# Kernel optimization log

Measured on AMD Instinct MI355X. Metric: run time of the kernel, lower is better.

## Reference

```python
import jax, jax.numpy as jnp
import numpy as np

D_MODEL, D_STATE, D_CONV, EXPAND = 2048, 16, 4, 2
D_INNER = D_MODEL * EXPAND
DT_RANK = D_MODEL // 16
B_SZ, SEQ = 2, 1024
WS = 0.02  # weight init scale for numerical stability


def setup_inputs() -> dict:
    key = jax.random.key(0)
    ks = jax.random.split(key, 14)
    rn = lambda k, s, sc=WS: jax.random.normal(k, s, dtype=jnp.float32) * sc
    return {
        "u": rn(ks[0], (B_SZ, SEQ, D_MODEL), 1.0),
        "w_in": rn(ks[1], (2 * D_INNER, D_MODEL)),
        "b_in": rn(ks[2], (2 * D_INNER,)),
        "w_out": rn(ks[3], (D_MODEL, D_INNER)),
        "b_out": rn(ks[4], (D_MODEL,)),
        "w_dt": rn(ks[5], (D_INNER, DT_RANK)),
        "b_dt": rn(ks[6], (D_INNER,)),
        "w_xdt": rn(ks[7], (DT_RANK, D_INNER)),
        "w_xb": rn(ks[8], (D_STATE, D_INNER)),
        "w_xc": rn(ks[9], (D_STATE, D_INNER)),
        "conv_w": rn(ks[10], (D_INNER, 1, D_CONV), 0.2),
        "conv_b": rn(ks[11], (D_INNER,), 0.1),
        "A_log": jnp.log(jax.random.uniform(ks[12], (D_INNER, D_STATE), minval=0.5, maxval=8.0)),
        "D_param": rn(ks[13], (D_INNER,), 1.0),
    }


def reference(u, w_in, b_in, w_out, b_out, w_dt, b_dt, w_xdt, w_xb, w_xc, conv_w, conv_b, A_log, D_param):
    B, L, _ = u.shape
    # in_proj and split into x, z   [B, L, D_INNER] each
    xz = u @ w_in.T + b_in
    x, z = jnp.split(xz, 2, axis=-1)
    # causal depthwise conv1d (torch pads both sides D_CONV-1 then slices [:L] == left pad)
    xt = x.transpose(0, 2, 1)  # [B, D_INNER, L]
    conv = jax.lax.conv_general_dilated(
        xt, conv_w, window_strides=(1,), padding=[(D_CONV - 1, 0)],
        feature_group_count=D_INNER, dimension_numbers=("NCH", "OIH", "NCH"))
    x = jax.nn.silu((conv + conv_b[None, :, None]).transpose(0, 2, 1))  # [B, L, D_INNER]
    # SSM parameters
    dt = jax.nn.softplus((x @ w_xdt.T) @ w_dt.T + b_dt)  # [B, L, D_INNER]
    Bm = x @ w_xb.T  # [B, L, D_STATE]
    Cm = x @ w_xc.T  # [B, L, D_STATE]
    A = -jnp.exp(A_log.astype(jnp.float32))  # [D_INNER, D_STATE]

    def step(h, inp):
        dt_t, B_t, C_t, x_t = inp  # [B,D_INNER], [B,N], [B,N], [B,D_INNER]
        dA = jnp.exp(dt_t[..., None] * A)                         # [B, D_INNER, N]
        h = h * dA + x_t[..., None] * (dt_t[..., None] * B_t[:, None, :])
        y = jnp.einsum("bdn,bn->bd", h, C_t) + D_param * x_t
        return h, y

    h0 = jnp.zeros((B, D_INNER, D_STATE), dtype=x.dtype)
    _, ys = jax.lax.scan(step, h0, (dt.transpose(1, 0, 2), Bm.transpose(1, 0, 2),
                                    Cm.transpose(1, 0, 2), x.transpose(1, 0, 2)))
    y = ys.transpose(1, 0, 2) * jax.nn.silu(z)  # [B, L, D_INNER]
    return y @ w_out.T + b_out
```

## Files before the change

### kernel.cpp

```cpp
#include <hip/hip_runtime.h>
#include <hip/hip_bf16.h>


#define DEV __device__ __forceinline__

typedef __attribute__((ext_vector_type(8))) __bf16 bf16x8;
typedef __attribute__((ext_vector_type(4))) float f32x4;
typedef unsigned int u32;

DEV float bf2f(__hip_bfloat16 x) { return __bfloat162float(x); }
DEV __hip_bfloat16 f2bf(float x) { return __float2bfloat16(x); }
DEV float bfu2f(unsigned short u) {
    union { u32 i; float f; } c; c.i = ((u32)u) << 16; return c.f;
}
DEV unsigned short f2bfu(float x) {
    __hip_bfloat16 h = __float2bfloat16(x);
    return *reinterpret_cast<unsigned short*>(&h);
}
DEV float softplusf(float v) { return v > 20.f ? v : log1pf(__expf(v)); }
DEV float siluf(float v) { return v / (1.f + __expf(-v)); }

DEV void storeOut(float* C, size_t off, float v) { C[off] = v; }
DEV void storeOut(__hip_bfloat16* C, size_t off, float v) { C[off] = f2bf(v); }

DEV void async16(void* lds, const void* g) {
    __builtin_amdgcn_global_load_lds(
        (const __attribute__((address_space(1))) u32*)(unsigned long long)g,
        (__attribute__((address_space(3))) u32*)(u32)(unsigned long long)lds,
        16, 0, 0);
}

template <int CTRL>
DEV float dppadd(float v) {
    int x = __builtin_amdgcn_update_dpp(
        0, __builtin_bit_cast(int, v), CTRL, 0xF, 0xF, true);
    return v + __builtin_bit_cast(float, x);
}

__global__ __launch_bounds__(512, 2) void gemm256_bt(
    const __hip_bfloat16* __restrict__ A, int lda,
    const __hip_bfloat16* __restrict__ W, int ldw,
    const float* __restrict__ bias,
    __hip_bfloat16* __restrict__ C, int ldc, int K)
{
    __shared__ __align__(16) unsigned short As[4][256 * 32];
    __shared__ __align__(16) unsigned short Bs[4][256 * 32];

    const int t    = threadIdx.x;
    const int nwg  = gridDim.x * gridDim.y;
    const int orig = blockIdx.y * gridDim.x + blockIdx.x;
    const int swz  = (orig & 7) * (nwg >> 3) + (orig >> 3);
    const int mBase = (swz / gridDim.x) * 256;
    const int nBase = (swz % gridDim.x) * 256;

    const int wave = t >> 6;
    const int lane = t & 63;
    const int wm   = (wave >> 2) * 128;
    const int wn   = (wave & 3) * 64;
    const int ln15 = lane & 15;
    const int quad = lane >> 4;
    const int kof  = quad * 8;

    f32x4 acc[8][4];
    const f32x4 vzero = {0.f, 0.f, 0.f, 0.f};
#pragma unroll
    for (int i = 0; i < 8; ++i)
#pragma unroll
        for (int j = 0; j < 4; ++j) acc[i][j] = vzero;

    auto stage = [&](int buf, int k0, int half) {
        const int idx = half * 512 + t;
        const int le  = (idx * 8) ^ (((idx >> 3) & 3) << 3);
        const int r   = le >> 5;
        const int c   = le & 31;
        async16(&As[buf][idx * 8], A + (size_t)(mBase + r) * lda + k0 + c);
        async16(&Bs[buf][idx * 8], W + (size_t)(nBase + r) * ldw + k0 + c);
    };

    const int NT = K >> 5;

#pragma unroll 1
    for (int p = 0; p < 3 && p < NT; ++p) {
        stage(p, p << 5, 0);
        stage(p, p << 5, 1);
    }

#pragma unroll 1
    for (int T = 0; T < NT; ++T) {
        const int buf = T & 3;
        if (T + 2 < NT)      asm volatile("s_waitcnt vmcnt(8)" ::: "memory");
        else if (T + 1 < NT) asm volatile("s_waitcnt vmcnt(4)" ::: "memory");
        else                 asm volatile("s_waitcnt vmcnt(0)" ::: "memory");
        __builtin_amdgcn_s_barrier();
        __builtin_amdgcn_sched_barrier(0);

        const unsigned short* __restrict__ Ab = As[buf];
        const unsigned short* __restrict__ Bb = Bs[buf];
        const int k0n  = (T + 3) << 5;
        const int bufn = (T + 3) & 3;

        bf16x8 af[4], bfr[4], af2[4];
#pragma unroll
        for (int i = 0; i < 4; ++i) {
            const int ra = wm + i * 16 + ln15;
            af[i] = *reinterpret_cast<const bf16x8*>(
                &Ab[(ra * 32 + kof) ^ (((ra >> 1) & 3) << 3)]);
            const int rb = wn + i * 16 + ln15;
            bfr[i] = *reinterpret_cast<const bf16x8*>(
                &Bb[(rb * 32 + kof) ^ (((rb >> 1) & 3) << 3)]);
        }
        if (T + 3 < NT) stage(bufn, k0n, 0);
        __builtin_amdgcn_s_barrier();
        __builtin_amdgcn_s_setprio(1);
#pragma unroll
        for (int i = 0; i < 4; ++i)
#pragma unroll
            for (int j = 0; j < 4; ++j)
                acc[i][j] = __builtin_amdgcn_mfma_f32_16x16x32_bf16(
                    af[i], bfr[j], acc[i][j], 0, 0, 0);
        __builtin_amdgcn_s_setprio(0);
        __builtin_amdgcn_sched_barrier(0);

#pragma unroll
        for (int i = 0; i < 4; ++i) {
            const int ra = wm + 64 + i * 16 + ln15;
            af2[i] = *reinterpret_cast<const bf16x8*>(
                &Ab[(ra * 32 + kof) ^ (((ra >> 1) & 3) << 3)]);
        }
        if (T + 3 < NT) stage(bufn, k0n, 1);
        __builtin_amdgcn_s_barrier();
        __builtin_amdgcn_s_setprio(1);
#pragma unroll
        for (int i = 0; i < 4; ++i)
#pragma unroll
            for (int j = 0; j < 4; ++j)
                acc[4 + i][j] = __builtin_amdgcn_mfma_f32_16x16x32_bf16(
                    af2[i], bfr[j], acc[4 + i][j], 0, 0, 0);
        __builtin_amdgcn_s_setprio(0);
        __builtin_amdgcn_sched_barrier(0);
    }

#pragma unroll
    for (int i = 0; i < 8; ++i) {
        const int gm = mBase + wm + i * 16 + quad * 4;
#pragma unroll
        for (int j = 0; j < 4; ++j) {
            const int gn = nBase + wn + j * 16 + ln15;
            const float bv = bias ? bias[gn] : 0.f;
#pragma unroll
            for (int r = 0; r < 4; ++r)
                C[(size_t)(gm + r) * ldc + gn] = f2bf(acc[i][j][r] + bv);
        }
    }
}

template <int ACT, typename OutT>
__global__ __launch_bounds__(256) void gemm_bt(
    const __hip_bfloat16* __restrict__ A, int lda,
    const __hip_bfloat16* __restrict__ W, int ldw,
    const float* __restrict__ bias,
    OutT* __restrict__ C, int ldc, int K)
{
    __shared__ __align__(16) unsigned short AsU[2][128 * 64];
    __shared__ __align__(16) unsigned short BsU[2][128 * 64];

    const int t     = threadIdx.x;
    const int mBase = blockIdx.y * 128;
    const int nBase = blockIdx.x * 128;
    const int wave  = t >> 6;
    const int lane  = t & 63;
    const int wm    = (wave >> 1) * 64;
    const int wn    = (wave & 1) * 64;
    const int ln15  = lane & 15;
    const int quad  = lane >> 4;

    f32x4 acc[4][4];
    const f32x4 vzero = {0.f, 0.f, 0.f, 0.f};
#pragma unroll
    for (int i = 0; i < 4; ++i)
#pragma unroll
        for (int j = 0; j < 4; ++j) acc[i][j] = vzero;

    auto stage = [&](int buf, int k0) {
#pragma unroll
        for (int i = 0; i < 4; ++i) {
            int idx = i * 256 + t;
            int r = idx >> 3;
            int c = (idx & 7) << 3;
            async16(&AsU[buf][idx * 8], A + (size_t)(mBase + r) * lda + k0 + c);
            async16(&BsU[buf][idx * 8], W + (size_t)(nBase + r) * ldw + k0 + c);
        }
    };

    const int nIter = K >> 6;
    stage(0, 0);

    for (int it = 0; it < nIter; ++it) {
        __syncthreads();
        if (it + 1 < nIter) stage((it + 1) & 1, (it + 1) << 6);
        const unsigned short* As = AsU[it & 1];
        const unsigned short* Bs = BsU[it & 1];

#pragma unroll
        for (int kk = 0; kk < 64; kk += 32) {
            const int kof = kk + quad * 8;
            bf16x8 af[4], bfr[4];
#pragma unroll
            for (int i = 0; i < 4; ++i) {
                af[i]  = *reinterpret_cast<const bf16x8*>(&As[(wm + i * 16 + ln15) * 64 + kof]);
                bfr[i] = *reinterpret_cast<const bf16x8*>(&Bs[(wn + i * 16 + ln15) * 64 + kof]);
            }
#pragma unroll
            for (int i = 0; i < 4; ++i)
#pragma unroll
                for (int j = 0; j < 4; ++j)
                    acc[i][j] = __builtin_amdgcn_mfma_f32_16x16x32_bf16(af[i], bfr[j], acc[i][j], 0, 0, 0);
        }
    }

#pragma unroll
    for (int i = 0; i < 4; ++i) {
        const int gm = mBase + wm + i * 16 + quad * 4;
#pragma unroll
        for (int j = 0; j < 4; ++j) {
            const int gn = nBase + wn + j * 16 + ln15;
            const float bv = bias ? bias[gn] : 0.f;
#pragma unroll
            for (int r = 0; r < 4; ++r) {
                float v = acc[i][j][r] + bv;
                if (ACT == 1) v = softplusf(v);
                storeOut(C, (size_t)(gm + r) * ldc + gn, v);
            }
        }
    }
}

__global__ __launch_bounds__(256) void gemm_bt_sk(
    const __hip_bfloat16* __restrict__ A, int lda,
    const __hip_bfloat16* __restrict__ W, int ldw,
    float* __restrict__ part, int ldc, int K, int slices, int sliceElems)
{
    __shared__ __align__(16) unsigned short AsU[2][128 * 64];
    __shared__ __align__(16) unsigned short BsU[2][128 * 64];

    const int t     = threadIdx.x;
    const int mBase = blockIdx.y * 128;
    const int nBase = blockIdx.x * 128;
    const int kLen  = K / slices;
    const int kOff  = blockIdx.z * kLen;
    const int wave  = t >> 6;
    const int lane  = t & 63;
    const int wm    = (wave >> 1) * 64;
    const int wn    = (wave & 1) * 64;
    const int ln15  = lane & 15;
    const int quad  = lane >> 4;

    f32x4 acc[4][4];
    const f32x4 vzero = {0.f, 0.f, 0.f, 0.f};
#pragma unroll
    for (int i = 0; i < 4; ++i)
#pragma unroll
        for (int j = 0; j < 4; ++j) acc[i][j] = vzero;

    auto stage = [&](int buf, int k0) {
#pragma unroll
        for (int i = 0; i < 4; ++i) {
            int idx = i * 256 + t;
            int r = idx >> 3;
            int c = (idx & 7) << 3;
            async16(&AsU[buf][idx * 8], A + (size_t)(mBase + r) * lda + k0 + c);
            async16(&BsU[buf][idx * 8], W + (size_t)(nBase + r) * ldw + k0 + c);
        }
    };

    const int nIter = kLen >> 6;
    stage(0, kOff);

    for (int it = 0; it < nIter; ++it) {
        __syncthreads();
        if (it + 1 < nIter) stage((it + 1) & 1, kOff + ((it + 1) << 6));
        const unsigned short* As = AsU[it & 1];
        const unsigned short* Bs = BsU[it & 1];

#pragma unroll
        for (int kk = 0; kk < 64; kk += 32) {
            const int kof = kk + quad * 8;
            bf16x8 af[4], bfr[4];
#pragma unroll
            for (int i = 0; i < 4; ++i) {
                af[i]  = *reinterpret_cast<const bf16x8*>(&As[(wm + i * 16 + ln15) * 64 + kof]);
                bfr[i] = *reinterpret_cast<const bf16x8*>(&Bs[(wn + i * 16 + ln15) * 64 + kof]);
            }
#pragma unroll
            for (int i = 0; i < 4; ++i)
#pragma unroll
                for (int j = 0; j < 4; ++j)
                    acc[i][j] = __builtin_amdgcn_mfma_f32_16x16x32_bf16(af[i], bfr[j], acc[i][j], 0, 0, 0);
        }
    }

    float* Cp = part + (size_t)blockIdx.z * sliceElems;
#pragma unroll
    for (int i = 0; i < 4; ++i) {
        const int gm = mBase + wm + i * 16 + quad * 4;
#pragma unroll
        for (int j = 0; j < 4; ++j) {
            const int gn = nBase + wn + j * 16 + ln15;
#pragma unroll
            for (int r = 0; r < 4; ++r)
                Cp[(size_t)(gm + r) * ldc + gn] = acc[i][j][r];
        }
    }
}

__global__ __launch_bounds__(256) void reduce_proj(
    const float* __restrict__ part, __hip_bfloat16* __restrict__ proj)
{
    int i = blockIdx.x * 256 + threadIdx.x;
    float s = 0.f;
#pragma unroll
    for (int z = 0; z < 8; ++z) s += part[(size_t)z * 524288 + i];
    proj[i] = f2bf(s);
}

__global__ __launch_bounds__(256) void cast_f32_bf16(
    const float* __restrict__ in, __hip_bfloat16* __restrict__ out)
{
    size_t i = ((size_t)blockIdx.x * 256 + threadIdx.x) * 8;
    const float4 a = *reinterpret_cast<const float4*>(in + i);
    const float4 b = *reinterpret_cast<const float4*>(in + i + 4);
    unsigned short r[8];
    r[0] = f2bfu(a.x); r[1] = f2bfu(a.y); r[2] = f2bfu(a.z); r[3] = f2bfu(a.w);
    r[4] = f2bfu(b.x); r[5] = f2bfu(b.y); r[6] = f2bfu(b.z); r[7] = f2bfu(b.w);
    *reinterpret_cast<uint4*>(out + i) = *reinterpret_cast<uint4*>(r);
}

__global__ __launch_bounds__(256) void build_wcat(
    const float* __restrict__ w_xdt,
    const float* __restrict__ w_xb,
    const float* __restrict__ w_xc,
    __hip_bfloat16* __restrict__ wcat)
{
    int tid = blockIdx.x * 256 + threadIdx.x;
    int r = tid >> 12;
    int c = tid & 4095;
    float v = 0.f;
    if (r < 128)      v = w_xdt[r * 4096 + c];
    else if (r < 144) v = w_xb[(r - 128) * 4096 + c];
    else if (r < 160) v = w_xc[(r - 144) * 4096 + c];
    wcat[tid] = f2bf(v);
}

__global__ __launch_bounds__(256) void conv_siluz(
    const __hip_bfloat16* __restrict__ xzr,
    __hip_bfloat16* __restrict__ xzw,
    const float* __restrict__ conv_w,
    const float* __restrict__ conv_b,
    __hip_bfloat16* __restrict__ xc)
{
    const int tid = blockIdx.x * 256 + threadIdx.x;
    if (tid < (1 << 20)) {
        const int row = tid >> 9;
        const int d8  = (tid & 511) << 3;
        const int l   = row & 1023;
        uint4 tv[4];
#pragma unroll
        for (int k = 0; k < 4; ++k) {
            const int ll = l - 3 + k;
            if (ll >= 0)
                tv[k] = *reinterpret_cast<const uint4*>(
                    &xzr[(size_t)(row - 3 + k) * 8192 + d8]);
            else
                tv[k] = make_uint4(0u, 0u, 0u, 0u);
        }
        const float4 b0 = *reinterpret_cast<const float4*>(&conv_b[d8]);
        const float4 b1 = *reinterpret_cast<const float4*>(&conv_b[d8 + 4]);
        const unsigned short* t0 = (const unsigned short*)&tv[0];
        const unsigned short* t1 = (const unsigned short*)&tv[1];
        const unsigned short* t2 = (const unsigned short*)&tv[2];
        const unsigned short* t3 = (const unsigned short*)&tv[3];
        unsigned short o[8];
#pragma unroll
        for (int j = 0; j < 8; ++j) {
            const float4 w = *reinterpret_cast<const float4*>(&conv_w[(d8 + j) * 4]);
            float acc = (j < 4) ? ((const float*)&b0)[j] : ((const float*)&b1)[j - 4];
            acc += bfu2f(t0[j]) * w.x;
            acc += bfu2f(t1[j]) * w.y;
            acc += bfu2f(t2[j]) * w.z;
            acc += bfu2f(t3[j]) * w.w;
            o[j] = f2bfu(siluf(acc));
        }
        *reinterpret_cast<uint4*>(&xc[(size_t)row * 4096 + d8]) =
            *reinterpret_cast<const uint4*>(o);
    } else {
        const int zi  = tid - (1 << 20);
        const int row = zi >> 9;
        const int d8  = (zi & 511) << 3;
        const size_t a = (size_t)row * 8192 + 4096 + d8;
        const uint4 v = *reinterpret_cast<const uint4*>(&xzr[a]);
        const unsigned short* zv = (const unsigned short*)&v;
        unsigned short o[8];
#pragma unroll
        for (int j = 0; j < 8; ++j)
            o[j] = f2bfu(siluf(bfu2f(zv[j])));
        *reinterpret_cast<uint4*>(&xzw[a]) = *reinterpret_cast<const uint4*>(o);
    }
}

#define SCAN_T 128
#define ST4 132
#define ST2 136

__global__ __launch_bounds__(256) void scan_kernel(
    const float* __restrict__ dt,
    __hip_bfloat16* xcyg,
    const __hip_bfloat16* __restrict__ proj,
    const __hip_bfloat16* __restrict__ xz,
    const float* __restrict__ A_log,
    const float* __restrict__ Dp)
{
    __shared__ __align__(16) float          s_dt[16 * ST4];
    __shared__ __align__(16) unsigned short s_x [16 * ST2];
    __shared__ __align__(16) unsigned short s_z [16 * ST2];
    __shared__ __align__(16) unsigned short s_B [16 * ST2];
    __shared__ __align__(16) unsigned short s_C [16 * ST2];
    __shared__ __align__(16) unsigned short s_y [16 * ST2];

    const int t   = threadIdx.x;
    const int g   = t >> 4;
    const int n   = t & 15;
    const int ch0 = blockIdx.x * 16;
    const int b   = ch0 >> 12;
    const int d0  = ch0 & 4095;
    const int d   = d0 + g;

    const float A2   = -__expf(A_log[d * 16 + n]) * 1.44269504f;
    const float Dpar = Dp[d];
    const size_t rowBase = (size_t)b * 1024;

    const int lrow = t >> 1;
    const int lh8  = (t & 1) << 3;
    const int dr0  = t >> 2,         dc0 = (t & 3) << 2;
    const int dr1  = (256 + t) >> 2, dc1 = ((256 + t) & 3) << 2;

    float4 rdt0, rdt1; uint4 rx, rz, rB, rC;
    auto load_chunk = [&](int t0) {
        rdt0 = *reinterpret_cast<const float4*>(&dt[(rowBase + t0 + dr0) * 4096 + d0 + dc0]);
        rdt1 = *reinterpret_cast<const float4*>(&dt[(rowBase + t0 + dr1) * 4096 + d0 + dc1]);
        rx = *reinterpret_cast<const uint4*>(&xcyg[(rowBase + t0 + lrow) * 4096 + d0 + lh8]);
        rz = *reinterpret_cast<const uint4*>(&xz[(rowBase + t0 + lrow) * 8192 + 4096 + d0 + lh8]);
        rB = *reinterpret_cast<const uint4*>(&proj[(rowBase + t0 + lrow) * 256 + 128 + lh8]);
        rC = *reinterpret_cast<const uint4*>(&proj[(rowBase + t0 + lrow) * 256 + 144 + lh8]);
    };

    load_chunk(0);
    float h = 0.f;

    for (int c = 0; c < 1024 / SCAN_T; ++c) {
        const int t0 = c * SCAN_T;
        __syncthreads();
        {
            const float* pd0 = (const float*)&rdt0;
            const float* pd1 = (const float*)&rdt1;
#pragma unroll
            for (int j = 0; j < 4; ++j) {
                s_dt[(dc0 + j) * ST4 + dr0] = pd0[j];
                s_dt[(dc1 + j) * ST4 + dr1] = pd1[j];
            }
            const unsigned short* px = (const unsigned short*)&rx;
            const unsigned short* pz = (const unsigned short*)&rz;
            const unsigned short* pB = (const unsigned short*)&rB;
            const unsigned short* pC = (const unsigned short*)&rC;
#pragma unroll
            for (int j = 0; j < 8; ++j) {
                s_x[(lh8 + j) * ST2 + lrow] = px[j];
                s_z[(lh8 + j) * ST2 + lrow] = pz[j];
                s_B[(lh8 + j) * ST2 + lrow] = pB[j];
                s_C[(lh8 + j) * ST2 + lrow] = pC[j];
            }
        }
        __syncthreads();
        if (c + 1 < 1024 / SCAN_T) load_chunk(t0 + SCAN_T);

#pragma unroll 1
        for (int l0 = 0; l0 < SCAN_T; l0 += 8) {
            const uint4 vx = *reinterpret_cast<const uint4*>(&s_x[g * ST2 + l0]);
            const uint4 vz = *reinterpret_cast<const uint4*>(&s_z[g * ST2 + l0]);
            const uint4 vB = *reinterpret_cast<const uint4*>(&s_B[n * ST2 + l0]);
            const uint4 vC = *reinterpret_cast<const uint4*>(&s_C[n * ST2 + l0]);
            const float4 vd0 = *reinterpret_cast<const float4*>(&s_dt[g * ST4 + l0]);
            const float4 vd1 = *reinterpret_cast<const float4*>(&s_dt[g * ST4 + l0 + 4]);
            const unsigned short* ux = (const unsigned short*)&vx;
            const unsigned short* uz = (const unsigned short*)&vz;
            const unsigned short* uB = (const unsigned short*)&vB;
            const unsigned short* uC = (const unsigned short*)&vC;
            const float* fd0 = (const float*)&vd0;
            const float* fd1 = (const float*)&vd1;
            unsigned short y8[8];
#pragma unroll
            for (int j = 0; j < 8; ++j) {
                const float dtv = (j < 4) ? fd0[j] : fd1[j - 4];
                const float xv  = bfu2f(ux[j]);
                const float Bn  = bfu2f(uB[j]);
                const float Cn  = bfu2f(uC[j]);
                const float e   = __builtin_amdgcn_exp2f(dtv * A2);
                h = fmaf(h, e, (xv * dtv) * Bn);
                float p = h * Cn;
                p = dppadd<0xB1>(p);
                p = dppadd<0x4E>(p);
                p = dppadd<0x141>(p);
                p = dppadd<0x140>(p);
                if (n == 0) {
                    const float zgv = bfu2f(uz[j]);
                    y8[j] = f2bfu((p + Dpar * xv) * zgv);
                }
            }
            if (n == 0)
                *reinterpret_cast<uint4*>(&s_y[g * ST2 + l0]) =
                    *reinterpret_cast<const uint4*>(y8);
        }
        __syncthreads();

        {
            unsigned short tmp[8];
#pragma unroll
            for (int j = 0; j < 8; ++j) tmp[j] = s_y[(lh8 + j) * ST2 + lrow];
            *reinterpret_cast<uint4*>(&xcyg[(rowBase + t0 + lrow) * 4096 + d0 + lh8]) =
                *reinterpret_cast<const uint4*>(tmp);
        }
    }
}

extern "C" void kernel_launch(void* const* d_in, const int* in_sizes, int n_in,
                              void* d_out, int out_size, void* d_ws, size_t ws_size,
                              hipStream_t stream)
{
    const float* u      = (const float*)d_in[0];
    const float* w_in   = (const float*)d_in[1];
    const float* b_in   = (const float*)d_in[2];
    const float* w_out  = (const float*)d_in[3];
    const float* b_out  = (const float*)d_in[4];
    const float* w_dt   = (const float*)d_in[5];
    const float* b_dt   = (const float*)d_in[6];
    const float* w_xdt  = (const float*)d_in[7];
    const float* w_xb   = (const float*)d_in[8];
    const float* w_xc   = (const float*)d_in[9];
    const float* conv_w = (const float*)d_in[10];
    const float* conv_b = (const float*)d_in[11];
    const float* A_log  = (const float*)d_in[12];
    const float* D_par  = (const float*)d_in[13];
    float* out = (float*)d_out;

    char* ws = (char*)d_ws;
    __hip_bfloat16* xz    = (__hip_bfloat16*)(ws);
    __hip_bfloat16* xc    = (__hip_bfloat16*)(ws + 33554432);
    __hip_bfloat16* u_bf  = (__hip_bfloat16*)(ws + 33554432);
    __hip_bfloat16* wcat  = (__hip_bfloat16*)(ws + 50331648);
    __hip_bfloat16* w_dt_bf = (__hip_bfloat16*)(ws + 50331648);
    __hip_bfloat16* proj  = (__hip_bfloat16*)(ws + 52428800);
    float*          dtb   = (float*)(ws + 53477376);
    __hip_bfloat16* w_in_bf  = (__hip_bfloat16*)(ws + 53477376);
    float*          projPart = (float*)(ws + 53477376);
    __hip_bfloat16* w_out_bf = (__hip_bfloat16*)(ws + 53477376);

    cast_f32_bf16<<<2048, 256, 0, stream>>>(u, u_bf);
    cast_f32_bf16<<<8192, 256, 0, stream>>>(w_in, w_in_bf);

    build_wcat<<<4096, 256, 0, stream>>>(w_xdt, w_xb, w_xc, wcat);

    gemm256_bt<<<dim3(32, 8), 512, 0, stream>>>(
        u_bf, 2048, w_in_bf, 2048, b_in, xz, 8192, 2048);

    conv_siluz<<<8192, 256, 0, stream>>>(xz, xz, conv_w, conv_b, xc);

    gemm_bt_sk<<<dim3(2, 16, 8), 256, 0, stream>>>(
        xc, 4096, wcat, 4096, projPart, 256, 4096, 8, 524288);
    reduce_proj<<<2048, 256, 0, stream>>>(projPart, proj);

    cast_f32_bf16<<<256, 256, 0, stream>>>(w_dt, w_dt_bf);

    gemm_bt<1, float><<<dim3(32, 16), 256, 0, stream>>>(
        proj, 256, w_dt_bf, 128, b_dt, dtb, 4096, 128);

    scan_kernel<<<512, 256, 0, stream>>>(dtb, xc, proj, xz, A_log, D_par);

    cast_f32_bf16<<<4096, 256, 0, stream>>>(w_out, w_out_bf);

    gemm_bt<0, float><<<dim3(16, 16), 256, 0, stream>>>(
        xc, 4096, w_out_bf, 4096, b_out, out, 2048, 4096);
}
```

Before: 502.6 us.

## Give each scan thread two SSM states and double channels per block

Each scan thread now carries two state elements (n0 and n0+8) as packed float2 math, so a block covers 32 channels with 8 lanes per channel instead of 16. This halves the cross-lane DPP reduction depth and the redundant per-channel dt/x loads, and lets the compiler use packed FMA/mul. The grid drops from 512 to 256 blocks, which cuts parallelism on a wide GPU and may leave CUs idle while the latency-bound recurrence runs.

```diff
diff --git a/kernel.cpp b/kernel.cpp
--- a/kernel.cpp
+++ b/kernel.cpp
@@ -6,6 +6,7 @@
 
 typedef __attribute__((ext_vector_type(8))) __bf16 bf16x8;
 typedef __attribute__((ext_vector_type(4))) float f32x4;
+typedef __attribute__((ext_vector_type(2))) float f32x2;
 typedef unsigned int u32;
 
 DEV float bf2f(__hip_bfloat16 x) { return __bfloat162float(x); }
@@ -419,64 +420,82 @@
     const float* __restrict__ A_log,
     const float* __restrict__ Dp)
 {
-    __shared__ __align__(16) float          s_dt[16 * ST4];
-    __shared__ __align__(16) unsigned short s_x [16 * ST2];
-    __shared__ __align__(16) unsigned short s_z [16 * ST2];
+    __shared__ __align__(16) float          s_dt[32 * ST4];
+    __shared__ __align__(16) unsigned short s_x [32 * ST2];
+    __shared__ __align__(16) unsigned short s_z [32 * ST2];
     __shared__ __align__(16) unsigned short s_B [16 * ST2];
     __shared__ __align__(16) unsigned short s_C [16 * ST2];
-    __shared__ __align__(16) unsigned short s_y [16 * ST2];
+    __shared__ __align__(16) unsigned short s_y [32 * ST2];
 
     const int t   = threadIdx.x;
-    const int g   = t >> 4;
-    const int n   = t & 15;
-    const int ch0 = blockIdx.x * 16;
+    const int g   = t >> 3;
+    const int n0  = t & 7;
+    const int ch0 = blockIdx.x * 32;
     const int b   = ch0 >> 12;
     const int d0  = ch0 & 4095;
     const int d   = d0 + g;
 
-    const float A2   = -__expf(A_log[d * 16 + n]) * 1.44269504f;
+    f32x2 A2;
+    A2.x = -__expf(A_log[d * 16 + n0]) * 1.44269504f;
+    A2.y = -__expf(A_log[d * 16 + n0 + 8]) * 1.44269504f;
     const float Dpar = Dp[d];
     const size_t rowBase = (size_t)b * 1024;
 
-    const int lrow = t >> 1;
-    const int lh8  = (t & 1) << 3;
-    const int dr0  = t >> 2,         dc0 = (t & 3) << 2;
-    const int dr1  = (256 + t) >> 2, dc1 = ((256 + t) & 3) << 2;
-
-    float4 rdt0, rdt1; uint4 rx, rz, rB, rC;
+    const int rD = t >> 3, cD = (t & 7) << 2;
+    const int rX = t >> 2, cX = (t & 3) << 3;
+    const int rB = t >> 1, cB = (t & 1) << 3;
+
+    float4 rdt[4]; uint4 rx[2], rz[2], rBv, rCv;
     auto load_chunk = [&](int t0) {
-        rdt0 = *reinterpret_cast<const float4*>(&dt[(rowBase + t0 + dr0) * 4096 + d0 + dc0]);
-        rdt1 = *reinterpret_cast<const float4*>(&dt[(rowBase + t0 + dr1) * 4096 + d0 + dc1]);
-        rx = *reinterpret_cast<const uint4*>(&xcyg[(rowBase + t0 + lrow) * 4096 + d0 + lh8]);
-        rz = *reinterpret_cast<const uint4*>(&xz[(rowBase + t0 + lrow) * 8192 + 4096 + d0 + lh8]);
-        rB = *reinterpret_cast<const uint4*>(&proj[(rowBase + t0 + lrow) * 256 + 128 + lh8]);
-        rC = *reinterpret_cast<const uint4*>(&proj[(rowBase + t0 + lrow) * 256 + 144 + lh8]);
+#pragma unroll
+        for (int i = 0; i < 4; ++i)
+            rdt[i] = *reinterpret_cast<const float4*>(
+                &dt[(rowBase + t0 + rD + i * 32) * 4096 + d0 + cD]);
+#pragma unroll
+        for (int i = 0; i < 2; ++i) {
+            rx[i] = *reinterpret_cast<const uint4*>(
+                &xcyg[(rowBase + t0 + rX + i * 64) * 4096 + d0 + cX]);
+            rz[i] = *reinterpret_cast<const uint4*>(
+                &xz[(rowBase + t0 + rX + i * 64) * 8192 + 4096 + d0 + cX]);
+        }
+        rBv = *reinterpret_cast<const uint4*>(
+            &proj[(rowBase + t0 + rB) * 256 + 128 + cB]);
+        rCv = *reinterpret_cast<const uint4*>(
+            &proj[(rowBase + t0 + rB) * 256 + 144 + cB]);
     };
 
     load_chunk(0);
-    float h = 0.f;
+    f32x2 h = {0.f, 0.f};
 
     for (int c = 0; c < 1024 / SCAN_T; ++c) {
         const int t0 = c * SCAN_T;
         __syncthreads();
         {
-            const float* pd0 = (const float*)&rdt0;
-            const float* pd1 = (const float*)&rdt1;
-#pragma unroll
-            for (int j = 0; j < 4; ++j) {
-                s_dt[(dc0 + j) * ST4 + dr0] = pd0[j];
-                s_dt[(dc1 + j) * ST4 + dr1] = pd1[j];
-            }
-            const unsigned short* px = (const unsigned short*)&rx;
-            const unsigned short* pz = (const unsigned short*)&rz;
-            const unsigned short* pB = (const unsigned short*)&rB;
-            const unsigned short* pC = (const unsigned short*)&rC;
-#pragma unroll
-            for (int j = 0; j < 8; ++j) {
-                s_x[(lh8 + j) * ST2 + lrow] = px[j];
-                s_z[(lh8 + j) * ST2 + lrow] = pz[j];
-                s_B[(lh8 + j) * ST2 + lrow] = pB[j];
-                s_C[(lh8 + j) * ST2 + lrow] = pC[j];
+#pragma unroll
+            for (int i = 0; i < 4; ++i) {
+                const float* p = (const float*)&rdt[i];
+#pragma unroll
+                for (int jj = 0; jj < 4; ++jj)
+                    s_dt[(cD + jj) * ST4 + rD + i * 32] = p[jj];
+            }
+#pragma unroll
+            for (int i = 0; i < 2; ++i) {
+                const unsigned short* px = (const unsigned short*)&rx[i];
+                const unsigned short* pz = (const unsigned short*)&rz[i];
+#pragma unroll
+                for (int jj = 0; jj < 8; ++jj) {
+                    s_x[(cX + jj) * ST2 + rX + i * 64] = px[jj];
+                    s_z[(cX + jj) * ST2 + rX + i * 64] = pz[jj];
+                }
+            }
+            {
+                const unsigned short* pB = (const unsigned short*)&rBv;
+                const unsigned short* pC = (const unsigned short*)&rCv;
+#pragma unroll
+                for (int jj = 0; jj < 8; ++jj) {
+                    s_B[(cB + jj) * ST2 + rB] = pB[jj];
+                    s_C[(cB + jj) * ST2 + rB] = pC[jj];
+                }
             }
         }
         __syncthreads();
@@ -484,16 +503,20 @@
 
 #pragma unroll 1
         for (int l0 = 0; l0 < SCAN_T; l0 += 8) {
-            const uint4 vx = *reinterpret_cast<const uint4*>(&s_x[g * ST2 + l0]);
-            const uint4 vz = *reinterpret_cast<const uint4*>(&s_z[g * ST2 + l0]);
-            const uint4 vB = *reinterpret_cast<const uint4*>(&s_B[n * ST2 + l0]);
-            const uint4 vC = *reinterpret_cast<const uint4*>(&s_C[n * ST2 + l0]);
             const float4 vd0 = *reinterpret_cast<const float4*>(&s_dt[g * ST4 + l0]);
             const float4 vd1 = *reinterpret_cast<const float4*>(&s_dt[g * ST4 + l0 + 4]);
-            const unsigned short* ux = (const unsigned short*)&vx;
-            const unsigned short* uz = (const unsigned short*)&vz;
-            const unsigned short* uB = (const unsigned short*)&vB;
-            const unsigned short* uC = (const unsigned short*)&vC;
+            const uint4 vx  = *reinterpret_cast<const uint4*>(&s_x[g * ST2 + l0]);
+            const uint4 vz  = *reinterpret_cast<const uint4*>(&s_z[g * ST2 + l0]);
+            const uint4 vB0 = *reinterpret_cast<const uint4*>(&s_B[n0 * ST2 + l0]);
+            const uint4 vB1 = *reinterpret_cast<const uint4*>(&s_B[(n0 + 8) * ST2 + l0]);
+            const uint4 vC0 = *reinterpret_cast<const uint4*>(&s_C[n0 * ST2 + l0]);
+            const uint4 vC1 = *reinterpret_cast<const uint4*>(&s_C[(n0 + 8) * ST2 + l0]);
+            const unsigned short* ux  = (const unsigned short*)&vx;
+            const unsigned short* uz  = (const unsigned short*)&vz;
+            const unsigned short* uB0 = (const unsigned short*)&vB0;
+            const unsigned short* uB1 = (const unsigned short*)&vB1;
+            const unsigned short* uC0 = (const unsigned short*)&vC0;
+            const unsigned short* uC1 = (const unsigned short*)&vC1;
             const float* fd0 = (const float*)&vd0;
             const float* fd1 = (const float*)&vd1;
             unsigned short y8[8];
@@ -501,32 +524,42 @@
             for (int j = 0; j < 8; ++j) {
                 const float dtv = (j < 4) ? fd0[j] : fd1[j - 4];
                 const float xv  = bfu2f(ux[j]);
-                const float Bn  = bfu2f(uB[j]);
-                const float Cn  = bfu2f(uC[j]);
-                const float e   = __builtin_amdgcn_exp2f(dtv * A2);
-                h = fmaf(h, e, (xv * dtv) * Bn);
-                float p = h * Cn;
+                f32x2 Bp; Bp.x = bfu2f(uB0[j]); Bp.y = bfu2f(uB1[j]);
+                f32x2 Cp; Cp.x = bfu2f(uC0[j]); Cp.y = bfu2f(uC1[j]);
+                const f32x2 dA = A2 * (f32x2){dtv, dtv};
+                f32x2 e;
+                e.x = __builtin_amdgcn_exp2f(dA.x);
+                e.y = __builtin_amdgcn_exp2f(dA.y);
+                const float xdt = xv * dtv;
+                const f32x2 tt = Bp * (f32x2){xdt, xdt};
+                h = __builtin_elementwise_fma(h, e, tt);
+                const f32x2 pp = h * Cp;
+                float p = pp.x + pp.y;
                 p = dppadd<0xB1>(p);
                 p = dppadd<0x4E>(p);
                 p = dppadd<0x141>(p);
-                p = dppadd<0x140>(p);
-                if (n == 0) {
+                if (n0 == 0) {
                     const float zgv = bfu2f(uz[j]);
                     y8[j] = f2bfu((p + Dpar * xv) * zgv);
                 }
             }
-            if (n == 0)
+            if (n0 == 0)
                 *reinterpret_cast<uint4*>(&s_y[g * ST2 + l0]) =
                     *reinterpret_cast<const uint4*>(y8);
         }
         __syncthreads();
 
         {
-            unsigned short tmp[8];
-#pragma unroll
-            for (int j = 0; j < 8; ++j) tmp[j] = s_y[(lh8 + j) * ST2 + lrow];
-            *reinterpret_cast<uint4*>(&xcyg[(rowBase + t0 + lrow) * 4096 + d0 + lh8]) =
-                *reinterpret_cast<const uint4*>(tmp);
+#pragma unroll
+            for (int i = 0; i < 2; ++i) {
+                unsigned short tmp[8];
+#pragma unroll
+                for (int jj = 0; jj < 8; ++jj)
+                    tmp[jj] = s_y[(cX + jj) * ST2 + rX + i * 64];
+                *reinterpret_cast<uint4*>(
+                    &xcyg[(rowBase + t0 + rX + i * 64) * 4096 + d0 + cX]) =
+                    *reinterpret_cast<const uint4*>(tmp);
+            }
         }
     }
 }
@@ -582,7 +615,7 @@
     gemm_bt<1, float><<<dim3(32, 16), 256, 0, stream>>>(
         proj, 256, w_dt_bf, 128, b_dt, dtb, 4096, 128);
 
-    scan_kernel<<<512, 256, 0, stream>>>(dtb, xc, proj, xz, A_log, D_par);
+    scan_kernel<<<256, 256, 0, stream>>>(dtb, xc, proj, xz, A_log, D_par);
 
     cast_f32_bf16<<<4096, 256, 0, stream>>>(w_out, w_out_bf);
 
```

New measurement: 555.0 us. +10.4%, slower.

## Fuse dt projection GEMM and softplus into scan kernel via MFMA

Applied to the files above, without the earlier changes.

Removes the separate dt GEMM launch and its fp32 dt buffer round-trip through global memory (2x1024x4096 floats). Each scan block now async-loads the proj low-rank slice and its 16 rows of w_dt into swizzled LDS, computes dt per chunk with bf16 MFMA, and applies a faster exp2/log-based softplus before the recurrence. In exchange, every channel block redoes the small rank-128 matmul for its own channels, LDS use grows by about 36KB, and an extra barrier is added per chunk.

```diff
diff --git a/kernel.cpp b/kernel.cpp
--- a/kernel.cpp
+++ b/kernel.cpp
@@ -19,6 +19,11 @@
 }
 DEV float softplusf(float v) { return v > 20.f ? v : log1pf(__expf(v)); }
 DEV float siluf(float v) { return v / (1.f + __expf(-v)); }
+DEV float softplus_fast(float v) {
+    if (v > 20.f) return v;
+    const float e = __builtin_amdgcn_exp2f(v * 1.44269504f);
+    return 0.69314718f * __builtin_amdgcn_logf(1.f + e);
+}
 
 DEV void storeOut(float* C, size_t off, float v) { C[off] = v; }
 DEV void storeOut(__hip_bfloat16* C, size_t off, float v) { C[off] = f2bf(v); }
@@ -412,10 +417,11 @@
 #define ST2 136
 
 __global__ __launch_bounds__(256) void scan_kernel(
-    const float* __restrict__ dt,
+    const __hip_bfloat16* __restrict__ proj,
     __hip_bfloat16* xcyg,
-    const __hip_bfloat16* __restrict__ proj,
     const __hip_bfloat16* __restrict__ xz,
+    const __hip_bfloat16* __restrict__ wdt,
+    const float* __restrict__ bdt,
     const float* __restrict__ A_log,
     const float* __restrict__ Dp)
 {
@@ -425,62 +431,115 @@
     __shared__ __align__(16) unsigned short s_B [16 * ST2];
     __shared__ __align__(16) unsigned short s_C [16 * ST2];
     __shared__ __align__(16) unsigned short s_y [16 * ST2];
-
-    const int t   = threadIdx.x;
-    const int g   = t >> 4;
-    const int n   = t & 15;
-    const int ch0 = blockIdx.x * 16;
-    const int b   = ch0 >> 12;
-    const int d0  = ch0 & 4095;
-    const int d   = d0 + g;
+    __shared__ __align__(16) unsigned short s_pa[128 * 128];
+    __shared__ __align__(16) unsigned short s_wd[16 * 128];
+
+    const int t    = threadIdx.x;
+    const int g    = t >> 4;
+    const int n    = t & 15;
+    const int wave = t >> 6;
+    const int lane = t & 63;
+    const int ln15 = lane & 15;
+    const int quad = lane >> 4;
+    const int wm32 = wave * 32;
+    const int ch0  = blockIdx.x * 16;
+    const int b    = ch0 >> 12;
+    const int d0   = ch0 & 4095;
+    const int d    = d0 + g;
 
     const float A2   = -__expf(A_log[d * 16 + n]) * 1.44269504f;
     const float Dpar = Dp[d];
     const size_t rowBase = (size_t)b * 1024;
+    const float bdtv = bdt[d0 + ln15];
+
+    {
+        const int idx = t;
+        const int le  = (idx * 8) ^ (((idx >> 4) & 7) << 3);
+        async16(&s_wd[idx * 8], &wdt[(size_t)(d0 + (idx >> 4)) * 128 + (le & 127)]);
+    }
 
     const int lrow = t >> 1;
     const int lh8  = (t & 1) << 3;
-    const int dr0  = t >> 2,         dc0 = (t & 3) << 2;
-    const int dr1  = (256 + t) >> 2, dc1 = ((256 + t) & 3) << 2;
-
-    float4 rdt0, rdt1; uint4 rx, rz, rB, rC;
+
+    uint4 rx, rz, rBv, rCv;
     auto load_chunk = [&](int t0) {
-        rdt0 = *reinterpret_cast<const float4*>(&dt[(rowBase + t0 + dr0) * 4096 + d0 + dc0]);
-        rdt1 = *reinterpret_cast<const float4*>(&dt[(rowBase + t0 + dr1) * 4096 + d0 + dc1]);
-        rx = *reinterpret_cast<const uint4*>(&xcyg[(rowBase + t0 + lrow) * 4096 + d0 + lh8]);
-        rz = *reinterpret_cast<const uint4*>(&xz[(rowBase + t0 + lrow) * 8192 + 4096 + d0 + lh8]);
-        rB = *reinterpret_cast<const uint4*>(&proj[(rowBase + t0 + lrow) * 256 + 128 + lh8]);
-        rC = *reinterpret_cast<const uint4*>(&proj[(rowBase + t0 + lrow) * 256 + 144 + lh8]);
+        rx  = *reinterpret_cast<const uint4*>(
+            &xcyg[(rowBase + t0 + lrow) * 4096 + d0 + lh8]);
+        rz  = *reinterpret_cast<const uint4*>(
+            &xz[(rowBase + t0 + lrow) * 8192 + 4096 + d0 + lh8]);
+        rBv = *reinterpret_cast<const uint4*>(
+            &proj[(rowBase + t0 + lrow) * 256 + 128 + lh8]);
+        rCv = *reinterpret_cast<const uint4*>(
+            &proj[(rowBase + t0 + lrow) * 256 + 144 + lh8]);
     };
 
     load_chunk(0);
     float h = 0.f;
 
+#pragma unroll 1
     for (int c = 0; c < 1024 / SCAN_T; ++c) {
         const int t0 = c * SCAN_T;
         __syncthreads();
+
+#pragma unroll
+        for (int s = 0; s < 8; ++s) {
+            const int idx = s * 256 + t;
+            const int le  = (idx * 8) ^ (((idx >> 4) & 7) << 3);
+            async16(&s_pa[idx * 8],
+                    &proj[(rowBase + t0 + (idx >> 4)) * 256 + (le & 127)]);
+        }
         {
-            const float* pd0 = (const float*)&rdt0;
-            const float* pd1 = (const float*)&rdt1;
-#pragma unroll
-            for (int j = 0; j < 4; ++j) {
-                s_dt[(dc0 + j) * ST4 + dr0] = pd0[j];
-                s_dt[(dc1 + j) * ST4 + dr1] = pd1[j];
-            }
             const unsigned short* px = (const unsigned short*)&rx;
             const unsigned short* pz = (const unsigned short*)&rz;
-            const unsigned short* pB = (const unsigned short*)&rB;
-            const unsigned short* pC = (const unsigned short*)&rC;
-#pragma unroll
-            for (int j = 0; j < 8; ++j) {
-                s_x[(lh8 + j) * ST2 + lrow] = px[j];
-                s_z[(lh8 + j) * ST2 + lrow] = pz[j];
-                s_B[(lh8 + j) * ST2 + lrow] = pB[j];
-                s_C[(lh8 + j) * ST2 + lrow] = pC[j];
+            const unsigned short* pB = (const unsigned short*)&rBv;
+            const unsigned short* pC = (const unsigned short*)&rCv;
+#pragma unroll
+            for (int jj = 0; jj < 8; ++jj) {
+                s_x[(lh8 + jj) * ST2 + lrow] = px[jj];
+                s_z[(lh8 + jj) * ST2 + lrow] = pz[jj];
+                s_B[(lh8 + jj) * ST2 + lrow] = pB[jj];
+                s_C[(lh8 + jj) * ST2 + lrow] = pC[jj];
             }
         }
         __syncthreads();
         if (c + 1 < 1024 / SCAN_T) load_chunk(t0 + SCAN_T);
+
+        {
+            f32x4 dacc[2];
+            const f32x4 vz4 = {0.f, 0.f, 0.f, 0.f};
+            dacc[0] = vz4; dacc[1] = vz4;
+#pragma unroll
+            for (int ks = 0; ks < 4; ++ks) {
+                const int kof = ks * 32 + quad * 8;
+                bf16x8 paf[2], wbf;
+#pragma unroll
+                for (int i = 0; i < 2; ++i) {
+                    const int ra = wm32 + i * 16 + ln15;
+                    paf[i] = *reinterpret_cast<const bf16x8*>(
+                        &s_pa[(ra * 128 + kof) ^ ((ra & 7) << 3)]);
+                }
+                {
+                    const int rb = ln15;
+                    wbf = *reinterpret_cast<const bf16x8*>(
+                        &s_wd[(rb * 128 + kof) ^ ((rb & 7) << 3)]);
+                }
+#pragma unroll
+                for (int i = 0; i < 2; ++i)
+                    dacc[i] = __builtin_amdgcn_mfma_f32_16x16x32_bf16(
+                        paf[i], wbf, dacc[i], 0, 0, 0);
+            }
+#pragma unroll
+            for (int i = 0; i < 2; ++i) {
+                const int tb = wm32 + i * 16 + quad * 4;
+                const int dd = ln15;
+                f32x4 w;
+#pragma unroll
+                for (int r = 0; r < 4; ++r)
+                    w[r] = softplus_fast(dacc[i][r] + bdtv);
+                *reinterpret_cast<f32x4*>(&s_dt[dd * ST4 + tb]) = w;
+            }
+        }
+        __syncthreads();
 
 #pragma unroll 1
         for (int l0 = 0; l0 < SCAN_T; l0 += 8) {
@@ -524,8 +583,9 @@
         {
             unsigned short tmp[8];
 #pragma unroll
-            for (int j = 0; j < 8; ++j) tmp[j] = s_y[(lh8 + j) * ST2 + lrow];
-            *reinterpret_cast<uint4*>(&xcyg[(rowBase + t0 + lrow) * 4096 + d0 + lh8]) =
+            for (int jj = 0; jj < 8; ++jj) tmp[jj] = s_y[(lh8 + jj) * ST2 + lrow];
+            *reinterpret_cast<uint4*>(
+                &xcyg[(rowBase + t0 + lrow) * 4096 + d0 + lh8]) =
                 *reinterpret_cast<const uint4*>(tmp);
         }
     }
@@ -558,7 +618,6 @@
     __hip_bfloat16* wcat  = (__hip_bfloat16*)(ws + 50331648);
     __hip_bfloat16* w_dt_bf = (__hip_bfloat16*)(ws + 50331648);
     __hip_bfloat16* proj  = (__hip_bfloat16*)(ws + 52428800);
-    float*          dtb   = (float*)(ws + 53477376);
     __hip_bfloat16* w_in_bf  = (__hip_bfloat16*)(ws + 53477376);
     float*          projPart = (float*)(ws + 53477376);
     __hip_bfloat16* w_out_bf = (__hip_bfloat16*)(ws + 53477376);
@@ -579,10 +638,8 @@
 
     cast_f32_bf16<<<256, 256, 0, stream>>>(w_dt, w_dt_bf);
 
-    gemm_bt<1, float><<<dim3(32, 16), 256, 0, stream>>>(
-        proj, 256, w_dt_bf, 128, b_dt, dtb, 4096, 128);
-
-    scan_kernel<<<512, 256, 0, stream>>>(dtb, xc, proj, xz, A_log, D_par);
+    scan_kernel<<<512, 256, 0, stream>>>(
+        proj, xc, xz, w_dt_bf, b_dt, A_log, D_par);
 
     cast_f32_bf16<<<4096, 256, 0, stream>>>(w_out, w_out_bf);
 
```

Measured after the change: 463.9 us. 7.7% less time.
